# Kernel optimization log

Hardware: AMD Instinct MI355X
Metric: run time of the kernel (lower is better)

Reference implementation:

```python
import jax, jax.numpy as jnp
import numpy as np

SEQ = 4096
BLOCK = 64
NUM_RAND = 3
B, H, D = 1, 12, 64


def _build_bigbird_mask(seq_len=SEQ, block=BLOCK, num_rand=NUM_RAND, seed=0):
    """Dense [S,S] BigBird mask: global first/last block, window +-1 block,
    num_rand random blocks per middle row (mirrors bigbird_block_rand_mask)."""
    nb = seq_len // block
    rng = np.random.RandomState(seed)
    m = np.zeros((nb, nb), dtype=np.int32)
    # global blocks (first & last block attend/are attended everywhere)
    m[0, :] = 1
    m[-1, :] = 1
    m[:, 0] = 1
    m[:, -1] = 1
    # sliding window of one block on each side
    idx = np.arange(nb)
    win = np.abs(idx[:, None] - idx[None, :]) <= 1
    m[win] = 1
    # random blocks for middle rows, excluding window and global columns
    for i in range(1, nb - 1):
        cand = np.array([j for j in range(1, nb - 1) if abs(j - i) > 1], dtype=np.int32)
        sel = rng.permutation(cand)[:num_rand]
        m[i, sel] = 1
    return np.kron(m, np.ones((block, block), dtype=np.int32))


def setup_inputs() -> dict:
    key = jax.random.key(0)
    kq, kk, kv = jax.random.split(key, 3)
    q = jax.random.normal(kq, (B, H, SEQ, D), dtype=jnp.float32)
    k = jax.random.normal(kk, (B, H, SEQ, D), dtype=jnp.float32)
    v = jax.random.normal(kv, (B, H, SEQ, D), dtype=jnp.float32)
    mask = jnp.asarray(_build_bigbird_mask(), dtype=jnp.int32)  # [S, S]
    return {"q": q, "k": k, "v": v, "mask": mask}


def reference(q, k, v, mask):
    # OriginalFullAttention with dense BigBird mask:
    # scores = QK^T / sqrt(D); masked positions get -10000 additive bias.
    scale = 1.0 / np.sqrt(D).astype(np.float32)
    scores = jnp.einsum("bhqd,bhkd->bhqk", q, k) * scale
    adder = (1.0 - mask.astype(scores.dtype)) * jnp.asarray(-10000.0, scores.dtype)
    probs = jax.nn.softmax(scores + adder[None, None, :, :], axis=-1)
    out = jnp.einsum("bhqk,bhkd->bhqd", probs, v)  # [B, H, S, D]
    return out
```

## Files before the change

kernel.cpp:

```cpp
#include <hip/hip_runtime.h>
#include <stdint.h>

#define SEQ 4096
#define DH  64
#define NB  64
#define NH  12

typedef float  f32x4   __attribute__((ext_vector_type(4)));
typedef float  f32x16  __attribute__((ext_vector_type(16)));
typedef short  s16x8   __attribute__((ext_vector_type(8)));
typedef unsigned short ushort_t;
typedef unsigned long long u64;

__device__ __forceinline__ unsigned short f2bf(float x){
    union { float f; unsigned u; } c; c.f = x;
    unsigned u = c.u;
    u += 0x7fffu + ((u >> 16) & 1u);
    return (unsigned short)(u >> 16);
}

__device__ __forceinline__ unsigned cvtpk(float lo, float hi){
    unsigned r;
    asm("v_cvt_pk_bf16_f32 %0, %1, %2" : "=v"(r) : "v"(lo), "v"(hi));
    return r;
}

__device__ __forceinline__ s16x8 pack8(f32x4 a, f32x4 b){
    s16x8 r;
#pragma unroll
    for (int i = 0; i < 4; ++i) { r[i] = (short)f2bf(a[i]); r[i+4] = (short)f2bf(b[i]); }
    return r;
}

__device__ __forceinline__ int swz(int row, int col){
    return row * 64 + (col ^ ((row & 7) << 3));
}

#define GLOAD_LDS(gp, lp) __builtin_amdgcn_global_load_lds( \
    (const __attribute__((address_space(1))) unsigned int*)(gp), \
    (__attribute__((address_space(3))) unsigned int*)(lp), 16, 0, 0)

#define KBF_OFF   0
#define VTB_OFF   6291456
#define PART_OFF  12582912
#define BMP_OFF   15777792
#define WS_NEED   15778304
#define SLOT_F    4160

__global__ __launch_bounds__(256) void bb_conv(
        const float* __restrict__ k, const float* __restrict__ v,
        const int* __restrict__ mask,
        ushort_t* __restrict__ kbf, ushort_t* __restrict__ vtb,
        u64* __restrict__ bmp)
{
    const int lin = blockIdx.x;
    const int job = (lin & 7) * 96 + (lin >> 3);
    const int h   = job >> 6;
    const int kb  = job & 63;
    const int tid = threadIdx.x;
    __shared__ float vls[64*65];

    if (h == 0 && tid < 64){
        bool a = mask[(size_t)(kb*64)*SEQ + tid*64] != 0;
        u64 bm = __ballot(a);
        if (tid == 0) bmp[kb] = bm;
    }

    const int j = tid >> 2, c = (tid & 3) * 16;
    const size_t gsrc = (size_t)h*SEQ*DH + (size_t)(kb*64 + j)*DH + c;
    const size_t tdst = ((size_t)h*NB + kb) * 4096;

    {
        f32x4 a0 = *(const f32x4*)(k + gsrc);
        f32x4 a1 = *(const f32x4*)(k + gsrc + 4);
        f32x4 a2 = *(const f32x4*)(k + gsrc + 8);
        f32x4 a3 = *(const f32x4*)(k + gsrc + 12);
        *(s16x8*)&kbf[tdst + swz(j, c    )] = pack8(a0, a1);
        *(s16x8*)&kbf[tdst + swz(j, c + 8)] = pack8(a2, a3);
    }
    {
        f32x4 b0 = *(const f32x4*)(v + gsrc);
        f32x4 b1 = *(const f32x4*)(v + gsrc + 4);
        f32x4 b2 = *(const f32x4*)(v + gsrc + 8);
        f32x4 b3 = *(const f32x4*)(v + gsrc + 12);
#pragma unroll
        for (int i = 0; i < 4; ++i){
            vls[j*65 + c + i     ] = b0[i];
            vls[j*65 + c + 4 + i ] = b1[i];
            vls[j*65 + c + 8 + i ] = b2[i];
            vls[j*65 + c + 12 + i] = b3[i];
        }
    }
    __syncthreads();
    {
        const int d = tid >> 2, jc = (tid & 3) * 16;
        s16x8 r0, r1;
#pragma unroll
        for (int i = 0; i < 8; ++i){
            r0[i] = (short)f2bf(vls[(jc + i    )*65 + d]);
            r1[i] = (short)f2bf(vls[(jc + i + 8)*65 + d]);
        }
        *(s16x8*)&vtb[tdst + swz(d, jc    )] = r0;
        *(s16x8*)&vtb[tdst + swz(d, jc + 8)] = r1;
    }
}

__global__ __launch_bounds__(256) void bb_main(
        const float* __restrict__ q,
        const ushort_t* __restrict__ kbf, const ushort_t* __restrict__ vtb,
        const u64* __restrict__ bmp,
        float* __restrict__ out, float* __restrict__ part)
{
    const int lin = blockIdx.x;
    const int job = (lin & 7) * 117 + (lin >> 3);
    const int h   = job / 78;
    const int x   = job - h * 78;

    int qb, wq = -1, sp = 0; u64 rmask;
    if (x < 62) { qb = x + 1; rmask = ~0ull; }
    else { int e = x - 62; wq = e >> 3; sp = e & 7; qb = wq ? 63 : 0; rmask = 0xFFull << (sp*8); }

    const int tid  = threadIdx.x;
    const int wave = tid >> 6;
    const int lane = tid & 63;
    const int l31  = lane & 31;
    const int hi   = lane >> 5;
    const int qh   = wave >> 1;
    const int kh   = wave & 1;

    __shared__ __align__(16) ushort_t KV[2][2][4096];
    __shared__ float lsm[64];

    const size_t hoff = (size_t)h * SEQ * DH;

    s16x8 qf[4];
    {
        const float sc = 0.125f * 1.4426950408889634f;
        const float* qp = q + hoff + (size_t)(qb*64 + qh*32 + l31) * DH + 8*hi;
#pragma unroll
        for (int c = 0; c < 4; ++c){
            f32x4 a = *(const f32x4*)(qp + c*16);
            f32x4 b = *(const f32x4*)(qp + c*16 + 4);
            a *= sc; b *= sc;
            qf[c] = pack8(a, b);
        }
    }

    u64 bits = bmp[qb] & rmask;

    const ushort_t* Kb = kbf + (size_t)h * (NB*4096);
    const ushort_t* Vb = vtb + (size_t)h * (NB*4096);

    f32x16 oa0 = {0.f}, oa1 = {0.f};
    float lp = 0.f;

    const int soff = wave*1024 + lane*16;
#define STAGE(gbase, lbase)                                          \
    {                                                                \
        const char* g0 = (const char*)(gbase) + soff;                \
        char*       l0 = (char*)(lbase) + wave*1024;                 \
        GLOAD_LDS(g0, l0);                                           \
        GLOAD_LDS(g0 + 4096, l0 + 4096);                             \
    }

    if (bits){
        const int n = __popcll(bits);
        u64 bpre = bits;

        int kb0 = __builtin_ctzll(bpre); bpre &= bpre - 1;
        STAGE(Kb + (size_t)kb0*4096, &KV[0][0][0]);
        STAGE(Vb + (size_t)kb0*4096, &KV[0][1][0]);

        int buf = 0;
        for (int t = 0; t < n; ++t){
            asm volatile("s_waitcnt vmcnt(0)" ::: "memory");
            __builtin_amdgcn_s_barrier();

            if (bpre){
                int kbn = __builtin_ctzll(bpre); bpre &= bpre - 1;
                STAGE(Kb + (size_t)kbn*4096, &KV[buf^1][0][0]);
                STAGE(Vb + (size_t)kbn*4096, &KV[buf^1][1][0]);
            }

            const ushort_t* Kt = &KV[buf][0][0];
            const ushort_t* Vt = &KV[buf][1][0];

            f32x16 sa = {0.f};
            __builtin_amdgcn_s_setprio(1);
#pragma unroll
            for (int c = 0; c < 4; ++c){
                s16x8 kf = *(const s16x8*)&Kt[swz(kh*32 + l31, c*16 + 8*hi)];
                sa = __builtin_amdgcn_mfma_f32_32x32x16_bf16(kf, qf[c], sa, 0, 0, 0);
            }
            __builtin_amdgcn_s_setprio(0);

            float p[16];
#pragma unroll
            for (int r = 0; r < 16; ++r){
                p[r] = __builtin_amdgcn_exp2f(sa[r]);
                lp += p[r];
            }

            s16x8 pa[2];
#pragma unroll
            for (int s = 0; s < 2; ++s){
                unsigned a1 = cvtpk(p[8*s+0], p[8*s+1]);
                unsigned b1 = cvtpk(p[8*s+4], p[8*s+5]);
                unsigned a2 = cvtpk(p[8*s+2], p[8*s+3]);
                unsigned b2 = cvtpk(p[8*s+6], p[8*s+7]);
                asm("v_permlane32_swap_b32 %0, %1" : "+v"(a1), "+v"(b1));
                asm("v_permlane32_swap_b32 %0, %1" : "+v"(a2), "+v"(b2));
                union { unsigned w[4]; s16x8 v; } u;
                u.w[0] = a1; u.w[1] = a2; u.w[2] = b1; u.w[3] = b2;
                pa[s] = u.v;
            }

            __builtin_amdgcn_s_setprio(1);
#pragma unroll
            for (int s = 0; s < 2; ++s){
                s16x8 v0 = *(const s16x8*)&Vt[swz(     l31, kh*32 + s*16 + 8*hi)];
                s16x8 v1 = *(const s16x8*)&Vt[swz(32 + l31, kh*32 + s*16 + 8*hi)];
                oa0 = __builtin_amdgcn_mfma_f32_32x32x16_bf16(pa[s], v0, oa0, 0, 0, 0);
                oa1 = __builtin_amdgcn_mfma_f32_32x32x16_bf16(pa[s], v1, oa1, 0, 0, 0);
            }
            __builtin_amdgcn_s_setprio(0);

            buf ^= 1;
        }
    }
#undef STAGE

    float lpf = lp + __shfl_xor(lp, 32);

    __syncthreads();
    float* msm = (float*)&KV[0][0][0];

    if (kh == 1){
#pragma unroll
        for (int r = 0; r < 16; ++r){
            const int o = (qh*32 + ((r&3) + 8*(r>>2) + 4*hi)) * 64;
            msm[o +      l31] = oa0[r];
            msm[o + 32 + l31] = oa1[r];
        }
        if (lane < 32) lsm[qh*32 + lane] = lpf;
    }
    __syncthreads();

    if (kh == 0){
#pragma unroll
        for (int r = 0; r < 16; ++r){
            const int o = (qh*32 + ((r&3) + 8*(r>>2) + 4*hi)) * 64;
            msm[o +      l31] += oa0[r];
            msm[o + 32 + l31] += oa1[r];
        }
        if (lane < 32){
            float lt = lpf + lsm[qh*32 + lane];
            lsm[qh*32 + lane] = (wq < 0) ? (lt > 0.f ? 1.0f / lt : 0.f) : lt;
        }
    }
    __syncthreads();

    const size_t obase = hoff + (size_t)(qb*64) * DH;

    if (wq < 0){
#pragma unroll
        for (int i = 0; i < 4; ++i){
            const int idx = i*1024 + tid*4;
            f32x4 vv = *(const f32x4*)&msm[idx];
            vv *= lsm[idx >> 6];
            *(f32x4*)&out[obase + idx] = vv;
        }
    } else {
        float* pp = part + ((size_t)(h*2 + wq)*8 + sp) * SLOT_F;
#pragma unroll
        for (int i = 0; i < 4; ++i){
            const int idx = i*1024 + tid*4;
            *(f32x4*)&pp[idx] = *(const f32x4*)&msm[idx];
        }
        if (tid < 64) pp[4096 + tid] = lsm[tid];
    }
}

__global__ __launch_bounds__(256) void bb_comb(
        const float* __restrict__ part, float* __restrict__ out)
{
    const int h = blockIdx.x >> 1, wq = blockIdx.x & 1;
    const int qb = wq ? 63 : 0;
    const int tid = threadIdx.x;
    const int i = tid >> 2, cg = (tid & 3) * 16;

    const float* base = part + (size_t)(h*2 + wq) * 8 * SLOT_F;
    f32x4 acc[4] = {{0,0,0,0},{0,0,0,0},{0,0,0,0},{0,0,0,0}};
    float ls = 0.f;
#pragma unroll
    for (int s = 0; s < 8; ++s){
        const float* p = base + (size_t)s * SLOT_F;
#pragma unroll
        for (int c4 = 0; c4 < 4; ++c4)
            acc[c4] += *(const f32x4*)(p + (size_t)i*DH + cg + c4*4);
        ls += p[4096 + i];
    }
    const float inv = ls > 0.f ? 1.0f / ls : 0.f;
    float* op = out + (size_t)h*SEQ*DH + (size_t)(qb*64 + i)*DH + cg;
#pragma unroll
    for (int c4 = 0; c4 < 4; ++c4){
        f32x4 r = acc[c4] * inv;
        *(f32x4*)(op + c4*4) = r;
    }
}

__global__ __launch_bounds__(256) void bb_attn_fb(
        const float* __restrict__ q, const float* __restrict__ k,
        const float* __restrict__ v, const int* __restrict__ mask,
        float* __restrict__ out)
{
    const int qb   = blockIdx.x;
    const int h    = blockIdx.y;
    const int tid  = threadIdx.x;
    const int wave = tid >> 6;
    const int lane = tid & 63;
    const int lrow = lane & 15;
    const int lgrp = lane >> 4;

    __shared__ __align__(16) ushort_t Kb[64*64];
    __shared__ __align__(16) ushort_t Vt[64*64];
    __shared__ __align__(16) ushort_t Pw[4][16*64];

    const size_t hoff = (size_t)h * SEQ * DH;
    const int qrow = qb*64 + wave*16 + lrow;
    const float* qp = q + hoff + (size_t)qrow * DH + lgrp*8;
    s16x8 qf[2];
#pragma unroll
    for (int kc = 0; kc < 2; ++kc){
        f32x4 a = *(const f32x4*)(qp + kc*32);
        f32x4 b = *(const f32x4*)(qp + kc*32 + 4);
        a *= 0.125f; b *= 0.125f;
        qf[kc] = pack8(a, b);
    }
    const f32x4 zero = {0.f,0.f,0.f,0.f};
    f32x4 oa[4] = {zero, zero, zero, zero};
    float m_run[4] = {-1e30f,-1e30f,-1e30f,-1e30f};
    float l_run[4] = {0.f,0.f,0.f,0.f};
    const int* mrow = mask + (size_t)(qb*64) * SEQ;
    const int kr  = tid >> 2, kcg  = tid & 3;
    const int j2  = tid >> 3, dgrp = tid & 7;

    for (int kb = 0; kb < NB; ++kb){
        if (mrow[kb*64] == 0) continue;
        __syncthreads();
        {
            const float* kp = k + hoff + (size_t)(kb*64 + kr) * DH + kcg*16;
            f32x4 a0 = *(const f32x4*)(kp);
            f32x4 a1 = *(const f32x4*)(kp+4);
            f32x4 a2 = *(const f32x4*)(kp+8);
            f32x4 a3 = *(const f32x4*)(kp+12);
            *(s16x8*)&Kb[(kr*64) + (kcg*16     ^ ((kr&7)<<3))] = pack8(a0, a1);
            *(s16x8*)&Kb[(kr*64) + ((kcg*16+8) ^ ((kr&7)<<3))] = pack8(a2, a3);
        }
        {
            const float* vp0 = v + hoff + (size_t)(kb*64 + 2*j2) * DH + dgrp*8;
            f32x4 b0 = *(const f32x4*)(vp0);
            f32x4 b1 = *(const f32x4*)(vp0+4);
            f32x4 b2 = *(const f32x4*)(vp0+DH);
            f32x4 b3 = *(const f32x4*)(vp0+DH+4);
            float r0[8] = {b0[0],b0[1],b0[2],b0[3],b1[0],b1[1],b1[2],b1[3]};
            float r1[8] = {b2[0],b2[1],b2[2],b2[3],b3[0],b3[1],b3[2],b3[3]};
#pragma unroll
            for (int i = 0; i < 8; ++i){
                int dd = (i + dgrp) & 7;
                int d  = dgrp*8 + dd;
                unsigned val = (unsigned)f2bf(r0[dd]) | ((unsigned)f2bf(r1[dd]) << 16);
                *(unsigned*)&Vt[(d*64) + (2*j2 ^ ((d&7)<<3))] = val;
            }
        }
        __syncthreads();
        f32x4 sa[4] = {zero, zero, zero, zero};
#pragma unroll
        for (int jt = 0; jt < 4; ++jt)
#pragma unroll
            for (int kc = 0; kc < 2; ++kc){
                int row = jt*16 + lrow, col = kc*32 + lgrp*8;
                s16x8 kf = *(const s16x8*)&Kb[row*64 + (col ^ ((row&7)<<3))];
                sa[jt] = __builtin_amdgcn_mfma_f32_16x16x32_bf16(qf[kc], kf, sa[jt], 0, 0, 0);
            }
        float fac[4];
#pragma unroll
        for (int r = 0; r < 4; ++r){
            float mx = fmaxf(fmaxf(sa[0][r], sa[1][r]), fmaxf(sa[2][r], sa[3][r]));
            mx = fmaxf(mx, __shfl_xor(mx, 1));
            mx = fmaxf(mx, __shfl_xor(mx, 2));
            mx = fmaxf(mx, __shfl_xor(mx, 4));
            mx = fmaxf(mx, __shfl_xor(mx, 8));
            float mn = fmaxf(m_run[r], mx);
            fac[r] = __expf(m_run[r] - mn);
            m_run[r] = mn;
        }
#pragma unroll
        for (int r = 0; r < 4; ++r){
            float p0 = __expf(sa[0][r] - m_run[r]);
            float p1 = __expf(sa[1][r] - m_run[r]);
            float p2 = __expf(sa[2][r] - m_run[r]);
            float p3 = __expf(sa[3][r] - m_run[r]);
            sa[0][r]=p0; sa[1][r]=p1; sa[2][r]=p2; sa[3][r]=p3;
            float sm = p0+p1+p2+p3;
            sm += __shfl_xor(sm, 1);
            sm += __shfl_xor(sm, 2);
            sm += __shfl_xor(sm, 4);
            sm += __shfl_xor(sm, 8);
            l_run[r] = l_run[r]*fac[r] + sm;
        }
#pragma unroll
        for (int dc = 0; dc < 4; ++dc)
#pragma unroll
            for (int r = 0; r < 4; ++r) oa[dc][r] *= fac[r];
#pragma unroll
        for (int jt = 0; jt < 4; ++jt)
#pragma unroll
            for (int r = 0; r < 4; ++r){
                int row = lgrp*4 + r, col = jt*16 + lrow;
                Pw[wave][row*64 + (col ^ ((row&7)<<3))] = f2bf(sa[jt][r]);
            }
        s16x8 pf0 = *(const s16x8*)&Pw[wave][lrow*64 + ((     lgrp*8) ^ ((lrow&7)<<3))];
        s16x8 pf1 = *(const s16x8*)&Pw[wave][lrow*64 + ((32 + lgrp*8) ^ ((lrow&7)<<3))];
#pragma unroll
        for (int dc = 0; dc < 4; ++dc){
            int row0 = dc*16 + lrow;
            s16x8 v0 = *(const s16x8*)&Vt[row0*64 + ((     lgrp*8) ^ ((row0&7)<<3))];
            s16x8 v1 = *(const s16x8*)&Vt[row0*64 + ((32 + lgrp*8) ^ ((row0&7)<<3))];
            oa[dc] = __builtin_amdgcn_mfma_f32_16x16x32_bf16(pf0, v0, oa[dc], 0, 0, 0);
            oa[dc] = __builtin_amdgcn_mfma_f32_16x16x32_bf16(pf1, v1, oa[dc], 0, 0, 0);
        }
    }
    float inv[4];
#pragma unroll
    for (int r = 0; r < 4; ++r) inv[r] = 1.0f / l_run[r];
    float* op = out + hoff + (size_t)(qb*64 + wave*16) * DH;
#pragma unroll
    for (int dc = 0; dc < 4; ++dc)
#pragma unroll
        for (int r = 0; r < 4; ++r)
            op[(size_t)(lgrp*4 + r) * DH + dc*16 + lrow] = oa[dc][r] * inv[r];
}

extern "C" void kernel_launch(void* const* d_in, const int* in_sizes, int n_in,
                              void* d_out, int out_size, void* d_ws, size_t ws_size,
                              hipStream_t stream)
{
    const float* q    = (const float*)d_in[0];
    const float* k    = (const float*)d_in[1];
    const float* v    = (const float*)d_in[2];
    const int*   mask = (const int*)d_in[3];
    float* out = (float*)d_out;

    if (ws_size < (size_t)WS_NEED){
        dim3 grid(NB, NH, 1);
        bb_attn_fb<<<grid, 256, 0, stream>>>(q, k, v, mask, out);
        return;
    }

    char* ws = (char*)d_ws;
    ushort_t* kbf = (ushort_t*)(ws + KBF_OFF);
    ushort_t* vtb = (ushort_t*)(ws + VTB_OFF);
    float*    prt = (float*)   (ws + PART_OFF);
    u64*      bmp = (u64*)     (ws + BMP_OFF);

    bb_conv<<<dim3(768, 1, 1), 256, 0, stream>>>(k, v, mask, kbf, vtb, bmp);
    bb_main<<<dim3(936, 1, 1), 256, 0, stream>>>(q, kbf, vtb, bmp, out, prt);
    bb_comb<<<dim3(24, 1, 1), 256, 0, stream>>>(prt, out);
}
```

Baseline: 36.60 us.

## Load V fragments directly from global in MFMA-ready layout, skip LDS staging

The V-transpose prep kernel now writes V in a fragment-major layout, so each lane can load its MFMA B-operand straight from global memory. The main loop no longer stages V into LDS. It issues direct per-lane global loads for the current block and double-buffers only K through LDS, which halves shared memory and LDS traffic. The trade-off is that global-load latency for V now sits inside the compute loop, hidden only by the QK^T MFMA and softmax work. The loop also always issues a K prefetch (of the first block again when no blocks remain), a redundant load.

```diff
diff --git a/kernel.cpp b/kernel.cpp
--- a/kernel.cpp
+++ b/kernel.cpp
@@ -100,8 +100,9 @@
             r0[i] = (short)f2bf(vls[(jc + i    )*65 + d]);
             r1[i] = (short)f2bf(vls[(jc + i + 8)*65 + d]);
         }
-        *(s16x8*)&vtb[tdst + swz(d, jc    )] = r0;
-        *(s16x8*)&vtb[tdst + swz(d, jc + 8)] = r1;
+        const int f0 = ((jc >> 5) << 2) + (((jc >> 4) & 1) << 1) + (d >> 5);
+        *(s16x8*)&vtb[tdst + f0*512 +       (d & 31)*8] = r0;
+        *(s16x8*)&vtb[tdst + f0*512 + 256 + (d & 31)*8] = r1;
     }
 }
 
@@ -128,7 +129,7 @@
     const int qh   = wave >> 1;
     const int kh   = wave & 1;
 
-    __shared__ __align__(16) ushort_t KV[2][2][4096];
+    __shared__ __align__(16) ushort_t KV[2][4096];
     __shared__ float lsm[64];
 
     const size_t hoff = (size_t)h * SEQ * DH;
@@ -165,25 +166,28 @@
 
     if (bits){
         const int n = __popcll(bits);
-        u64 bpre = bits;
-
-        int kb0 = __builtin_ctzll(bpre); bpre &= bpre - 1;
-        STAGE(Kb + (size_t)kb0*4096, &KV[0][0][0]);
-        STAGE(Vb + (size_t)kb0*4096, &KV[0][1][0]);
-
+        u64 rem = bits;
+
+        const int kb0 = __builtin_ctzll(rem); rem &= rem - 1;
+        STAGE(Kb + (size_t)kb0*4096, &KV[0][0]);
+
+        int kb_cur = kb0;
         int buf = 0;
         for (int t = 0; t < n; ++t){
             asm volatile("s_waitcnt vmcnt(0)" ::: "memory");
             __builtin_amdgcn_s_barrier();
 
-            if (bpre){
-                int kbn = __builtin_ctzll(bpre); bpre &= bpre - 1;
-                STAGE(Kb + (size_t)kbn*4096, &KV[buf^1][0][0]);
-                STAGE(Vb + (size_t)kbn*4096, &KV[buf^1][1][0]);
-            }
-
-            const ushort_t* Kt = &KV[buf][0][0];
-            const ushort_t* Vt = &KV[buf][1][0];
+            const ushort_t* vp = Vb + (size_t)kb_cur*4096 + kh*2048 + lane*8;
+            s16x8 vf00 = *(const s16x8*)(vp       );
+            s16x8 vf01 = *(const s16x8*)(vp +  512);
+            s16x8 vf10 = *(const s16x8*)(vp + 1024);
+            s16x8 vf11 = *(const s16x8*)(vp + 1536);
+
+            int kbn = kb0;
+            if (rem){ kbn = __builtin_ctzll(rem); rem &= rem - 1; }
+            STAGE(Kb + (size_t)kbn*4096, &KV[buf^1][0]);
+
+            const ushort_t* Kt = &KV[buf][0];
 
             f32x16 sa = {0.f};
             __builtin_amdgcn_s_setprio(1);
@@ -216,15 +220,13 @@
             }
 
             __builtin_amdgcn_s_setprio(1);
-#pragma unroll
-            for (int s = 0; s < 2; ++s){
-                s16x8 v0 = *(const s16x8*)&Vt[swz(     l31, kh*32 + s*16 + 8*hi)];
-                s16x8 v1 = *(const s16x8*)&Vt[swz(32 + l31, kh*32 + s*16 + 8*hi)];
-                oa0 = __builtin_amdgcn_mfma_f32_32x32x16_bf16(pa[s], v0, oa0, 0, 0, 0);
-                oa1 = __builtin_amdgcn_mfma_f32_32x32x16_bf16(pa[s], v1, oa1, 0, 0, 0);
-            }
+            oa0 = __builtin_amdgcn_mfma_f32_32x32x16_bf16(pa[0], vf00, oa0, 0, 0, 0);
+            oa1 = __builtin_amdgcn_mfma_f32_32x32x16_bf16(pa[0], vf01, oa1, 0, 0, 0);
+            oa0 = __builtin_amdgcn_mfma_f32_32x32x16_bf16(pa[1], vf10, oa0, 0, 0, 0);
+            oa1 = __builtin_amdgcn_mfma_f32_32x32x16_bf16(pa[1], vf11, oa1, 0, 0, 0);
             __builtin_amdgcn_s_setprio(0);
 
+            kb_cur = kbn;
             buf ^= 1;
         }
     }
@@ -233,7 +235,7 @@
     float lpf = lp + __shfl_xor(lp, 32);
 
     __syncthreads();
-    float* msm = (float*)&KV[0][0][0];
+    float* msm = (float*)&KV[0][0];
 
     if (kh == 1){
 #pragma unroll
```

New measurement: 36.14 us. No clear change (-1.3%).
